# Kernel optimization log

Measured on AMD Instinct MI355X. Metric: run time of the kernel, lower is better.

## Reference

```python
import jax, jax.numpy as jnp
import numpy as np

GRID_SEGMENTS = [(15050, 15850, 0.2), (15870, 16440, 0.2), (16475, 17100, 0.2),
                 (4700, 4930, 0.05), (5630, 5880, 0.05), (6420, 6800, 0.05), (7500, 7920, 0.05)]

LATENT_DIM = 128
LAYERS = [512, 1024, 2048, 4096]
BATCH = 64
N_OBS = 4096


def make_wavelength_grid():
    segs = []
    for start, end, step in GRID_SEGMENTS:
        n = int(round((end - start) / step)) + 1  # torch.arange(start, end+step, step) length
        segs.append(start + step * np.arange(n, dtype=np.float64))
    return np.concatenate(segs).astype(np.float32)


def setup_inputs() -> dict:
    key = jax.random.key(0)
    grid = jnp.asarray(make_wavelength_grid())          # [N_hi] = [35582]
    output_dim = grid.shape[0]
    dims = [LATENT_DIM] + LAYERS + [output_dim]
    keys = jax.random.split(key, len(dims) + 2)
    inp = {}
    a = 0.2
    for i in range(len(dims) - 1):
        fan_in, fan_out = dims[i], dims[i + 1]
        # kaiming_normal fan_out, leaky_relu(0.2): std = sqrt(2/(1+a^2)/fan_out)
        std = np.sqrt(2.0 / (1.0 + a * a) / fan_out)
        inp[f"W{i}"] = jax.random.normal(keys[i], (fan_out, fan_in), dtype=jnp.float32) * std
        inp[f"b{i}"] = jnp.zeros((fan_out,), dtype=jnp.float32)
    inp["z"] = jax.random.normal(keys[-2], (BATCH, LATENT_DIM), dtype=jnp.float32)
    lo, hi = 4700.0, 17100.0
    inp["observed_wavelengths"] = lo + (hi - lo) * jax.random.uniform(keys[-1], (BATCH, N_OBS), dtype=jnp.float32)
    inp["high_res_wavelength"] = grid
    return inp


def _interp1d(grid, spectrum, obs):
    # grid: [N] (concatenated segments, not globally sorted) ; spectrum: [B, N] ; obs: [B, M]
    perm = jnp.argsort(grid)
    g = grid[perm]                                  # sorted grid [N]
    s = spectrum[:, perm]                           # spectrum aligned to sorted grid [B, N]
    idx = jnp.clip(jnp.searchsorted(g, obs), 1, g.shape[0] - 1)  # [B, M]
    x0 = g[idx - 1]
    x1 = g[idx]
    y0 = jnp.take_along_axis(s, idx - 1, axis=1)
    y1 = jnp.take_along_axis(s, idx, axis=1)
    t = (obs - x0) / (x1 - x0)
    return y0 + t * (y1 - y0)


def reference(z, observed_wavelengths, high_res_wavelength,
              W0, b0, W1, b1, W2, b2, W3, b3, W4, b4):
    h = z
    for W, b in ((W0, b0), (W1, b1), (W2, b2), (W3, b3)):
        h = jax.nn.leaky_relu(h @ W.T + b, negative_slope=0.2)
    high_res_spectrum = h @ W4.T + b4               # [B, 35582]
    return _interp1d(high_res_wavelength, high_res_spectrum, observed_wavelengths)
```

## Files before the change

kernel.cpp:

```cpp
#include <hip/hip_runtime.h>


#define NOUT   35582
#define BATCH  64
#define NOBS   4096
#define ROT    25604
#define HIOFF  9978

typedef __bf16 bf16_t;
typedef __attribute__((ext_vector_type(8))) __bf16 bf16x8;
typedef __attribute__((ext_vector_type(4))) float f32x4;

__device__ __forceinline__ int sorted_to_orig(int p) {
    return (p < ROT) ? (p + HIOFF) : (p - ROT);
}

__global__ __launch_bounds__(256) void fc_kernel(
    const float* __restrict__ A, const float* __restrict__ W,
    const float* __restrict__ bias, float* __restrict__ out,
    bf16_t* __restrict__ out_bf, int K, int N)
{
    __shared__ float As[32][68];
    __shared__ float Bs[32][68];

    const int t  = threadIdx.x;
    const int n0 = blockIdx.x * 64;
    const int tx = t & 15;
    const int ty = t >> 4;

    float acc[4][4] = {};

    for (int k0 = 0; k0 < K; k0 += 32) {
        __syncthreads();
#pragma unroll
        for (int f = 0; f < 2; ++f) {
            int e  = (t + 256 * f) * 4;
            int m  = e >> 5;
            int kk = e & 31;
            float4 v = *(const float4*)(A + (size_t)m * K + k0 + kk);
            As[kk + 0][m] = v.x; As[kk + 1][m] = v.y;
            As[kk + 2][m] = v.z; As[kk + 3][m] = v.w;
        }
#pragma unroll
        for (int f = 0; f < 2; ++f) {
            int e  = (t + 256 * f) * 4;
            int n  = e >> 5;
            int kk = e & 31;
            float4 v = *(const float4*)(W + (size_t)(n0 + n) * K + k0 + kk);
            Bs[kk + 0][n] = v.x; Bs[kk + 1][n] = v.y;
            Bs[kk + 2][n] = v.z; Bs[kk + 3][n] = v.w;
        }
        __syncthreads();
#pragma unroll
        for (int kk = 0; kk < 32; ++kk) {
            float4 av = *(const float4*)&As[kk][ty * 4];
            float4 bv = *(const float4*)&Bs[kk][tx * 4];
            float a[4] = {av.x, av.y, av.z, av.w};
            float b[4] = {bv.x, bv.y, bv.z, bv.w};
#pragma unroll
            for (int i = 0; i < 4; ++i)
#pragma unroll
                for (int j = 0; j < 4; ++j) acc[i][j] += a[i] * b[j];
        }
    }

#pragma unroll
    for (int i = 0; i < 4; ++i) {
        int m = ty * 4 + i;
#pragma unroll
        for (int j = 0; j < 4; ++j) {
            int n = n0 + tx * 4 + j;
            float v = acc[i][j] + bias[n];
            v = v > 0.0f ? v : 0.2f * v;
            out[(size_t)m * N + n] = v;
            if (out_bf) out_bf[(size_t)m * N + n] = (bf16_t)v;
        }
    }
}

__global__ __launch_bounds__(256) void init_spec_kernel(
    const float* __restrict__ b, float* __restrict__ spec)
{
    int n = blockIdx.x * 256 + threadIdx.x;
    int m = blockIdx.y;
    if (n < NOUT) spec[(size_t)m * NOUT + n] = b[n];
}

__global__ __launch_bounds__(256) void build_sorted_kernel(
    const float* __restrict__ grid, float* __restrict__ gs)
{
    int p = blockIdx.x * 256 + threadIdx.x;
    if (p < NOUT) gs[p] = grid[sorted_to_orig(p)];
}

__global__ __launch_bounds__(256) void layer4_kernel(
    const bf16_t* __restrict__ Abf, const float* __restrict__ W,
    float* __restrict__ spec)
{
    const int lane = threadIdx.x & 63;
    const int wave = threadIdx.x >> 6;
    const int c16  = lane & 15;
    const int quad = lane >> 4;
    const int n    = blockIdx.x * 64 + wave * 16 + c16;
    const int nc   = n < NOUT ? n : NOUT - 1;
    const int kb   = blockIdx.y * 2048;

    const float*  wp = W   + (size_t)nc * 4096 + kb + quad * 8;
    const bf16_t* ap = Abf + (size_t)c16 * 4096 + kb + quad * 8;

    f32x4 acc[4] = {};

    for (int s = 0; s < 64; ++s) {
        float4 w0 = *(const float4*)(wp);
        float4 w1 = *(const float4*)(wp + 4);
        wp += 32;
        bf16x8 bv;
        bv[0] = (bf16_t)w0.x; bv[1] = (bf16_t)w0.y;
        bv[2] = (bf16_t)w0.z; bv[3] = (bf16_t)w0.w;
        bv[4] = (bf16_t)w1.x; bv[5] = (bf16_t)w1.y;
        bv[6] = (bf16_t)w1.z; bv[7] = (bf16_t)w1.w;
#pragma unroll
        for (int mt = 0; mt < 4; ++mt) {
            bf16x8 av = *(const bf16x8*)(ap + (size_t)mt * 16 * 4096 + s * 32);
            acc[mt] = __builtin_amdgcn_mfma_f32_16x16x32_bf16(av, bv, acc[mt], 0, 0, 0);
        }
    }

    if (n < NOUT) {
#pragma unroll
        for (int mt = 0; mt < 4; ++mt)
#pragma unroll
            for (int r = 0; r < 4; ++r) {
                int m = mt * 16 + quad * 4 + r;
                atomicAdd(&spec[(size_t)m * NOUT + n], acc[mt][r]);
            }
    }
}

__global__ __launch_bounds__(256) void interp_kernel(
    const float* __restrict__ gs, const float* __restrict__ spec,
    const float* __restrict__ obs, float* __restrict__ out)
{
    int idx = blockIdx.x * 256 + threadIdx.x;
    if (idx >= BATCH * NOBS) return;
    int m = idx >> 12;
    float x = obs[idx];

    int lo = 0, hi = NOUT;
    while (lo < hi) {
        int mid = (lo + hi) >> 1;
        if (gs[mid] < x) lo = mid + 1; else hi = mid;
    }
    int j = lo < 1 ? 1 : (lo > NOUT - 1 ? NOUT - 1 : lo);

    int o0 = sorted_to_orig(j - 1), o1 = sorted_to_orig(j);
    float x0 = gs[j - 1], x1 = gs[j];
    const float* sp = spec + (size_t)m * NOUT;
    float y0 = sp[o0], y1 = sp[o1];
    float t = (x - x0) / (x1 - x0);
    out[idx] = y0 + t * (y1 - y0);
}

extern "C" void kernel_launch(void* const* d_in, const int* in_sizes, int n_in,
                              void* d_out, int out_size, void* d_ws, size_t ws_size,
                              hipStream_t stream)
{
    const float* W0 = (const float*)d_in[0];
    const float* b0 = (const float*)d_in[1];
    const float* W1 = (const float*)d_in[2];
    const float* b1 = (const float*)d_in[3];
    const float* W2 = (const float*)d_in[4];
    const float* b2 = (const float*)d_in[5];
    const float* W3 = (const float*)d_in[6];
    const float* b3 = (const float*)d_in[7];
    const float* W4 = (const float*)d_in[8];
    const float* b4 = (const float*)d_in[9];
    const float* z  = (const float*)d_in[10];
    const float* obs  = (const float*)d_in[11];
    const float* grid = (const float*)d_in[12];
    float* out = (float*)d_out;

    char* ws = (char*)d_ws;
    float*  h1   = (float*)(ws);
    float*  h2   = (float*)(ws + 131072);
    float*  h3   = (float*)(ws + 393216);
    float*  h4   = (float*)(ws + 917504);
    bf16_t* h4b  = (bf16_t*)(ws + 1966080);
    float*  gs   = (float*)(ws + 2490368);
    float*  spec = (float*)(ws + 2632704);

    fc_kernel<<<dim3(512 / 64),  256, 0, stream>>>(z,  W0, b0, h1, nullptr, 128,  512);
    fc_kernel<<<dim3(1024 / 64), 256, 0, stream>>>(h1, W1, b1, h2, nullptr, 512,  1024);
    fc_kernel<<<dim3(2048 / 64), 256, 0, stream>>>(h2, W2, b2, h3, nullptr, 1024, 2048);
    fc_kernel<<<dim3(4096 / 64), 256, 0, stream>>>(h3, W3, b3, h4, h4b,     2048, 4096);

    build_sorted_kernel<<<dim3((NOUT + 255) / 256), 256, 0, stream>>>(grid, gs);
    init_spec_kernel<<<dim3((NOUT + 255) / 256, BATCH), 256, 0, stream>>>(b4, spec);

    layer4_kernel<<<dim3((NOUT + 63) / 64, 2), 256, 0, stream>>>(h4b, W4, spec);

    interp_kernel<<<dim3((BATCH * NOBS + 255) / 256), 256, 0, stream>>>(gs, spec, obs, out);
}
```

Baseline: 1.087 ms.

## Split-K the hidden FC layers and drop split-K atomics in final layer

The hidden-layer GEMMs are split along K across extra blocks, with partial sums written to a workspace and reduced by a new epilogue kernel that applies bias, leaky ReLU and bf16 conversion. This targets the very low block counts (8 to 64 blocks) of the small FC layers. The final layer stops splitting K and instead writes bias plus accumulator directly, which removes the bias-init kernel and the atomics. The trade-off is half as many blocks on the large final layer, plus extra launches and partial-sum traffic for the hidden layers.

```diff
diff --git a/kernel.cpp b/kernel.cpp
--- a/kernel.cpp
+++ b/kernel.cpp
@@ -9,28 +9,29 @@
 
 typedef __bf16 bf16_t;
 typedef __attribute__((ext_vector_type(8))) __bf16 bf16x8;
+typedef __attribute__((ext_vector_type(4))) __bf16 bf16x4;
 typedef __attribute__((ext_vector_type(4))) float f32x4;
 
 __device__ __forceinline__ int sorted_to_orig(int p) {
     return (p < ROT) ? (p + HIOFF) : (p - ROT);
 }
 
-__global__ __launch_bounds__(256) void fc_kernel(
+__global__ __launch_bounds__(256) void fc_gemm(
     const float* __restrict__ A, const float* __restrict__ W,
-    const float* __restrict__ bias, float* __restrict__ out,
-    bf16_t* __restrict__ out_bf, int K, int N)
+    float* __restrict__ part, int K, int N, int KC)
 {
     __shared__ float As[32][68];
     __shared__ float Bs[32][68];
 
     const int t  = threadIdx.x;
     const int n0 = blockIdx.x * 64;
+    const int kbase = blockIdx.y * KC;
     const int tx = t & 15;
     const int ty = t >> 4;
 
     float acc[4][4] = {};
 
-    for (int k0 = 0; k0 < K; k0 += 32) {
+    for (int k0 = kbase; k0 < kbase + KC; k0 += 32) {
         __syncthreads();
 #pragma unroll
         for (int f = 0; f < 2; ++f) {
@@ -64,26 +65,40 @@
         }
     }
 
+    float* p = part + (size_t)blockIdx.y * 64 * N;
 #pragma unroll
     for (int i = 0; i < 4; ++i) {
         int m = ty * 4 + i;
 #pragma unroll
-        for (int j = 0; j < 4; ++j) {
-            int n = n0 + tx * 4 + j;
-            float v = acc[i][j] + bias[n];
-            v = v > 0.0f ? v : 0.2f * v;
-            out[(size_t)m * N + n] = v;
-            if (out_bf) out_bf[(size_t)m * N + n] = (bf16_t)v;
-        }
-    }
-}
-
-__global__ __launch_bounds__(256) void init_spec_kernel(
-    const float* __restrict__ b, float* __restrict__ spec)
-{
-    int n = blockIdx.x * 256 + threadIdx.x;
-    int m = blockIdx.y;
-    if (n < NOUT) spec[(size_t)m * NOUT + n] = b[n];
+        for (int j = 0; j < 4; ++j)
+            p[(size_t)m * N + n0 + tx * 4 + j] = acc[i][j];
+    }
+}
+
+__global__ __launch_bounds__(256) void fc_epi(
+    const float* __restrict__ part, const float* __restrict__ bias,
+    float* __restrict__ out, bf16_t* __restrict__ out_bf, int N, int S)
+{
+    int idx = (blockIdx.x * 256 + threadIdx.x) * 4;
+    int n = idx & (N - 1);
+    float4 v = make_float4(0.f, 0.f, 0.f, 0.f);
+    for (int s = 0; s < S; ++s) {
+        float4 p = *(const float4*)(part + (size_t)s * 64 * N + idx);
+        v.x += p.x; v.y += p.y; v.z += p.z; v.w += p.w;
+    }
+    float4 b = *(const float4*)(bias + n);
+    v.x += b.x; v.y += b.y; v.z += b.z; v.w += b.w;
+    v.x = v.x > 0.f ? v.x : 0.2f * v.x;
+    v.y = v.y > 0.f ? v.y : 0.2f * v.y;
+    v.z = v.z > 0.f ? v.z : 0.2f * v.z;
+    v.w = v.w > 0.f ? v.w : 0.2f * v.w;
+    if (out) *(float4*)(out + idx) = v;
+    if (out_bf) {
+        bf16x4 o;
+        o[0] = (bf16_t)v.x; o[1] = (bf16_t)v.y;
+        o[2] = (bf16_t)v.z; o[3] = (bf16_t)v.w;
+        *(bf16x4*)(out_bf + idx) = o;
+    }
 }
 
 __global__ __launch_bounds__(256) void build_sorted_kernel(
@@ -95,7 +110,7 @@
 
 __global__ __launch_bounds__(256) void layer4_kernel(
     const bf16_t* __restrict__ Abf, const float* __restrict__ W,
-    float* __restrict__ spec)
+    const float* __restrict__ bias, float* __restrict__ spec)
 {
     const int lane = threadIdx.x & 63;
     const int wave = threadIdx.x >> 6;
@@ -103,14 +118,13 @@
     const int quad = lane >> 4;
     const int n    = blockIdx.x * 64 + wave * 16 + c16;
     const int nc   = n < NOUT ? n : NOUT - 1;
-    const int kb   = blockIdx.y * 2048;
-
-    const float*  wp = W   + (size_t)nc * 4096 + kb + quad * 8;
-    const bf16_t* ap = Abf + (size_t)c16 * 4096 + kb + quad * 8;
+
+    const float*  wp = W   + (size_t)nc * 4096 + quad * 8;
+    const bf16_t* ap = Abf + (size_t)c16 * 4096 + quad * 8;
 
     f32x4 acc[4] = {};
 
-    for (int s = 0; s < 64; ++s) {
+    for (int s = 0; s < 128; ++s) {
         float4 w0 = *(const float4*)(wp);
         float4 w1 = *(const float4*)(wp + 4);
         wp += 32;
@@ -127,12 +141,13 @@
     }
 
     if (n < NOUT) {
+        float b = bias[n];
 #pragma unroll
         for (int mt = 0; mt < 4; ++mt)
 #pragma unroll
             for (int r = 0; r < 4; ++r) {
                 int m = mt * 16 + quad * 4 + r;
-                atomicAdd(&spec[(size_t)m * NOUT + n], acc[mt][r]);
+                spec[(size_t)m * NOUT + n] = acc[mt][r] + b;
             }
     }
 }
@@ -184,20 +199,23 @@
     float*  h1   = (float*)(ws);
     float*  h2   = (float*)(ws + 131072);
     float*  h3   = (float*)(ws + 393216);
-    float*  h4   = (float*)(ws + 917504);
-    bf16_t* h4b  = (bf16_t*)(ws + 1966080);
-    float*  gs   = (float*)(ws + 2490368);
-    float*  spec = (float*)(ws + 2632704);
-
-    fc_kernel<<<dim3(512 / 64),  256, 0, stream>>>(z,  W0, b0, h1, nullptr, 128,  512);
-    fc_kernel<<<dim3(1024 / 64), 256, 0, stream>>>(h1, W1, b1, h2, nullptr, 512,  1024);
-    fc_kernel<<<dim3(2048 / 64), 256, 0, stream>>>(h2, W2, b2, h3, nullptr, 1024, 2048);
-    fc_kernel<<<dim3(4096 / 64), 256, 0, stream>>>(h3, W3, b3, h4, h4b,     2048, 4096);
+    bf16_t* h4b  = (bf16_t*)(ws + 917504);
+    float*  part = (float*)(ws + 1441792);
+    float*  gs   = (float*)(ws + 9830400);
+    float*  spec = (float*)(ws + 9973760);
 
     build_sorted_kernel<<<dim3((NOUT + 255) / 256), 256, 0, stream>>>(grid, gs);
-    init_spec_kernel<<<dim3((NOUT + 255) / 256, BATCH), 256, 0, stream>>>(b4, spec);
-
-    layer4_kernel<<<dim3((NOUT + 63) / 64, 2), 256, 0, stream>>>(h4b, W4, spec);
+
+    fc_gemm<<<dim3(8, 4),   256, 0, stream>>>(z,  W0, part, 128,  512,  32);
+    fc_epi <<<dim3(512 * 64 / 1024),  256, 0, stream>>>(part, b0, h1, nullptr, 512, 4);
+    fc_gemm<<<dim3(16, 8),  256, 0, stream>>>(h1, W1, part, 512,  1024, 64);
+    fc_epi <<<dim3(1024 * 64 / 1024), 256, 0, stream>>>(part, b1, h2, nullptr, 1024, 8);
+    fc_gemm<<<dim3(32, 8),  256, 0, stream>>>(h2, W2, part, 1024, 2048, 128);
+    fc_epi <<<dim3(2048 * 64 / 1024), 256, 0, stream>>>(part, b2, h3, nullptr, 2048, 8);
+    fc_gemm<<<dim3(64, 8),  256, 0, stream>>>(h3, W3, part, 2048, 4096, 256);
+    fc_epi <<<dim3(4096 * 64 / 1024), 256, 0, stream>>>(part, b3, nullptr, h4b, 4096, 8);
+
+    layer4_kernel<<<dim3((NOUT + 63) / 64), 256, 0, stream>>>(h4b, W4, b4, spec);
 
     interp_kernel<<<dim3((BATCH * NOBS + 255) / 256), 256, 0, stream>>>(gs, spec, obs, out);
 }
```

New measurement: 974.9 us. -10.3%, faster.
